# Optimization experiments

Measured on AMD Instinct MI355X. Metric: run time of the kernel, lower is better.

Reference implementation:

```python
import jax, jax.numpy as jnp
import numpy as np

B, M, D = 2048, 1024, 64
NEG_INF = -1e30


def setup_inputs() -> dict:
    key = jax.random.key(0)
    ks = jax.random.split(key, 12)
    s = 0.1  # small init scale for weights
    x = jax.random.normal(ks[0], (B, M, 4), dtype=jnp.float32)
    pad_mask = jax.random.bernoulli(ks[1], 0.1, (B, M))  # True = padded point
    return {
        "x": x,
        "pad_mask": pad_mask,
        "W_in": s * jax.random.normal(ks[2], (4, D), dtype=jnp.float32),
        "b_in": jnp.zeros((D,), jnp.float32),
        "seed": s * jax.random.normal(ks[3], (D,), dtype=jnp.float32),
        "Wq": s * jax.random.normal(ks[4], (D, D), dtype=jnp.float32),
        "Wk": s * jax.random.normal(ks[5], (D, D), dtype=jnp.float32),
        "Wv": s * jax.random.normal(ks[6], (D, D), dtype=jnp.float32),
        "Wo": s * jax.random.normal(ks[7], (D, D), dtype=jnp.float32),
        "b_o": jnp.zeros((D,), jnp.float32),
        "w_loc": s * jax.random.normal(ks[8], (D + 4, 1), dtype=jnp.float32),
        "b_loc": jnp.zeros((1,), jnp.float32),
        "prelu_a": jnp.full((1,), 0.25, jnp.float32),  # PReLU default slope
    }


def _wnet_global(x, pad_mask, W_in, b_in, seed, Wq, Wk, Wv, Wo, b_o):
    # Set-transformer style attention pooling -> one embedding per set [B, D]
    h = x @ W_in + b_in                                  # [B, M, D]
    q = seed @ Wq                                        # [D]
    k = h @ Wk                                           # [B, M, D]
    v = h @ Wv                                           # [B, M, D]
    scores = jnp.einsum("d,bmd->bm", q, k) / jnp.sqrt(jnp.float32(D))
    scores = jnp.where(pad_mask, NEG_INF, scores)
    attn = jax.nn.softmax(scores, axis=-1)               # [B, M]
    pooled = jnp.einsum("bm,bmd->bd", attn, v)           # [B, D]
    return pooled @ Wo + b_o                             # [B, D]


def reference(x, pad_mask, W_in, b_in, seed, Wq, Wk, Wv, Wo, b_o, w_loc, b_loc, prelu_a):
    feat = _wnet_global(x, pad_mask, W_in, b_in, seed, Wq, Wk, Wv, Wo, b_o)  # [B, D]
    # WNet_local: Linear on concat([x, feat]) split into two matmuls (same math,
    # avoids materializing the [B, M, D+4] concat)
    z = x @ w_loc[:4] + (feat @ w_loc[4:])[:, None, :] + b_loc               # [B, M, 1]
    w = jnp.where(z >= 0, z, prelu_a * z)[..., 0]                            # PReLU, [B, M]
    w = jnp.where(pad_mask, 0.0, w)
    # WLS: A = [-los, 1], r = residuals; diag(w) @ A == w[...,None] * A
    A = jnp.concatenate([-x[:, :, 1:4], jnp.ones((B, M, 1), x.dtype)], axis=-1)  # [B, M, 4]
    r = x[:, :, 0:1]                                                             # [B, M, 1]
    WA = w[:, :, None] * A
    Wr = w[:, :, None] * r
    out = (jnp.linalg.pinv(WA) @ Wr)[..., 0]                                     # [B, 4]
    return out
```

## Files before the change

### kernel.cpp

```cpp
#include <hip/hip_runtime.h>
#include <math.h>

#define BB 2048
#define MM 1024
#define DD 64
#define NEG_INF_F (-1e30f)

__device__ __forceinline__ float wredsum(float v) {
#pragma unroll
  for (int o = 32; o > 0; o >>= 1) v += __shfl_down(v, o);
  return v;
}
__device__ __forceinline__ float wredmax(float v) {
#pragma unroll
  for (int o = 32; o > 0; o >>= 1) v = fmaxf(v, __shfl_down(v, o));
  return v;
}

__global__ __launch_bounds__(256) void wls_fused(
    const float* __restrict__ x,
    const int*   __restrict__ pad,
    const float* __restrict__ W_in,
    const float* __restrict__ b_in,
    const float* __restrict__ seed,
    const float* __restrict__ Wq,
    const float* __restrict__ Wk,
    const float* __restrict__ Wv,
    const float* __restrict__ Wo,
    const float* __restrict__ b_o,
    const float* __restrict__ w_loc,
    const float* __restrict__ b_loc,
    const float* __restrict__ prelu_a,
    float* __restrict__ out)
{
  const int tid  = threadIdx.x;
  const int b    = blockIdx.x;
  const int wave = tid >> 6;
  const int lane = tid & 63;

  __shared__ float qv[DD], kqv[DD], hb[DD], pooledv[DD], featv[DD];
  __shared__ float c4s[5];
  __shared__ float rbuf[4][16];
  __shared__ float bcast[8];

  const float4* x4 = (const float4*)(x + (size_t)b * MM * 4);
  float4 xr[4];
  int mk[4];
#pragma unroll
  for (int k2 = 0; k2 < 4; ++k2) {
    xr[k2] = x4[tid + 256 * k2];
    mk[k2] = pad[(size_t)b * MM + tid + 256 * k2];
  }

  if (tid < DD) {
    float acc = 0.f;
    for (int e = 0; e < DD; ++e) acc += seed[e] * Wq[e * DD + tid];
    qv[tid] = acc;
  }
  __syncthreads();
  if (tid < DD) {
    float acc = 0.f;
    for (int d = 0; d < DD; ++d) acc += Wk[tid * DD + d] * qv[d];
    kqv[tid] = acc;
  }
  __syncthreads();
  if (tid < 4) {
    float acc = 0.f;
    for (int e = 0; e < DD; ++e) acc += W_in[tid * DD + e] * kqv[e];
    c4s[tid] = acc;
  } else if (tid == 4) {
    float acc = 0.f;
    for (int e = 0; e < DD; ++e) acc += b_in[e] * kqv[e];
    c4s[4] = acc;
  }
  __syncthreads();

  const float c40 = c4s[0], c41 = c4s[1], c42 = c4s[2], c43 = c4s[3], c0 = c4s[4];

  float sc[4];
  float pmax = -INFINITY;
#pragma unroll
  for (int k2 = 0; k2 < 4; ++k2) {
    float s = (xr[k2].x * c40 + xr[k2].y * c41 + xr[k2].z * c42 + xr[k2].w * c43 + c0) * 0.125f;
    if (mk[k2]) s = NEG_INF_F;
    sc[k2] = s;
    pmax = fmaxf(pmax, s);
  }
  pmax = wredmax(pmax);
  if (lane == 0) rbuf[wave][0] = pmax;
  __syncthreads();
  const float smax = fmaxf(fmaxf(rbuf[0][0], rbuf[1][0]), fmaxf(rbuf[2][0], rbuf[3][0]));
  __syncthreads();

  float se = 0.f, sx0 = 0.f, sx1 = 0.f, sx2 = 0.f, sx3 = 0.f;
#pragma unroll
  for (int k2 = 0; k2 < 4; ++k2) {
    float e = expf(sc[k2] - smax);
    se += e;
    sx0 += e * xr[k2].x; sx1 += e * xr[k2].y; sx2 += e * xr[k2].z; sx3 += e * xr[k2].w;
  }
  {
    float v5[5] = {se, sx0, sx1, sx2, sx3};
#pragma unroll
    for (int j = 0; j < 5; ++j) {
      float r = wredsum(v5[j]);
      if (lane == 0) rbuf[wave][j] = r;
    }
  }
  __syncthreads();
  if (tid < 5) bcast[tid] = rbuf[0][tid] + rbuf[1][tid] + rbuf[2][tid] + rbuf[3][tid];
  __syncthreads();

  if (tid < DD) {
    const float Z = bcast[0];
    const float xb0 = bcast[1] / Z, xb1 = bcast[2] / Z, xb2 = bcast[3] / Z, xb3 = bcast[4] / Z;
    hb[tid] = xb0 * W_in[tid] + xb1 * W_in[DD + tid] + xb2 * W_in[2 * DD + tid] +
              xb3 * W_in[3 * DD + tid] + b_in[tid];
  }
  __syncthreads();
  if (tid < DD) {
    float acc = 0.f;
    for (int e = 0; e < DD; ++e) acc += hb[e] * Wv[e * DD + tid];
    pooledv[tid] = acc;
  }
  __syncthreads();
  if (tid < DD) {
    float acc = 0.f;
    for (int e = 0; e < DD; ++e) acc += pooledv[e] * Wo[e * DD + tid];
    featv[tid] = acc + b_o[tid];
  }
  __syncthreads();
  if (wave == 0) {
    float p = featv[lane] * w_loc[4 + lane];
    p = wredsum(p);
    if (lane == 0) bcast[5] = p + b_loc[0];
  }
  __syncthreads();

  const float sB = bcast[5];
  const float aP = prelu_a[0];
  const float wl0 = w_loc[0], wl1 = w_loc[1], wl2 = w_loc[2], wl3 = w_loc[3];

  float g0 = 0.f, g1 = 0.f, g2 = 0.f, g3 = 0.f, g4 = 0.f, g5 = 0.f, g6 = 0.f,
        g7 = 0.f, g8 = 0.f, g9 = 0.f, r0 = 0.f, r1 = 0.f, r2 = 0.f, r3 = 0.f;
#pragma unroll
  for (int k2 = 0; k2 < 4; ++k2) {
    const float x0 = xr[k2].x, x1 = xr[k2].y, x2 = xr[k2].z, x3 = xr[k2].w;
    float z = x0 * wl0 + x1 * wl1 + x2 * wl2 + x3 * wl3 + sB;
    float w = (z >= 0.f) ? z : aP * z;
    if (mk[k2]) w = 0.f;
    const float w2 = w * w;
    g0 += w2 * x1 * x1; g1 += w2 * x1 * x2; g2 += w2 * x1 * x3; g3 -= w2 * x1;
    g4 += w2 * x2 * x2; g5 += w2 * x2 * x3; g6 -= w2 * x2;
    g7 += w2 * x3 * x3; g8 -= w2 * x3;
    g9 += w2;
    r0 -= w2 * x1 * x0; r1 -= w2 * x2 * x0; r2 -= w2 * x3 * x0; r3 += w2 * x0;
  }
  {
    float vals[14] = {g0, g1, g2, g3, g4, g5, g6, g7, g8, g9, r0, r1, r2, r3};
#pragma unroll
    for (int j = 0; j < 14; ++j) {
      float r = wredsum(vals[j]);
      if (lane == 0) rbuf[wave][j] = r;
    }
  }
  __syncthreads();

  if (tid == 0) {
    double s14[14];
#pragma unroll
    for (int j = 0; j < 14; ++j)
      s14[j] = (double)rbuf[0][j] + (double)rbuf[1][j] +
               (double)rbuf[2][j] + (double)rbuf[3][j];
    double G[4][5];
    G[0][0] = s14[0]; G[0][1] = s14[1]; G[0][2] = s14[2]; G[0][3] = s14[3]; G[0][4] = s14[10];
    G[1][0] = s14[1]; G[1][1] = s14[4]; G[1][2] = s14[5]; G[1][3] = s14[6]; G[1][4] = s14[11];
    G[2][0] = s14[2]; G[2][1] = s14[5]; G[2][2] = s14[7]; G[2][3] = s14[8]; G[2][4] = s14[12];
    G[3][0] = s14[3]; G[3][1] = s14[6]; G[3][2] = s14[8]; G[3][3] = s14[9]; G[3][4] = s14[13];

    for (int c = 0; c < 4; ++c) {
      int p = c; double mv = fabs(G[c][c]);
      for (int rr = c + 1; rr < 4; ++rr)
        if (fabs(G[rr][c]) > mv) { mv = fabs(G[rr][c]); p = rr; }
      if (p != c)
        for (int j = c; j < 5; ++j) { double t = G[c][j]; G[c][j] = G[p][j]; G[p][j] = t; }
      const double inv = 1.0 / G[c][c];
      for (int rr = c + 1; rr < 4; ++rr) {
        const double f = G[rr][c] * inv;
        for (int j = c; j < 5; ++j) G[rr][j] -= f * G[c][j];
      }
    }
    double y[4];
    for (int c = 3; c >= 0; --c) {
      double acc = G[c][4];
      for (int j = c + 1; j < 4; ++j) acc -= G[c][j] * y[j];
      y[c] = acc / G[c][c];
    }
    float4 o;
    o.x = (float)y[0]; o.y = (float)y[1]; o.z = (float)y[2]; o.w = (float)y[3];
    *(float4*)(out + (size_t)b * 4) = o;
  }
}

extern "C" void kernel_launch(void* const* d_in, const int* in_sizes, int n_in,
                              void* d_out, int out_size, void* d_ws, size_t ws_size,
                              hipStream_t stream) {
  const float* x       = (const float*)d_in[0];
  const int*   pad     = (const int*)d_in[1];
  const float* W_in    = (const float*)d_in[2];
  const float* b_in    = (const float*)d_in[3];
  const float* seed    = (const float*)d_in[4];
  const float* Wq      = (const float*)d_in[5];
  const float* Wk      = (const float*)d_in[6];
  const float* Wv      = (const float*)d_in[7];
  const float* Wo      = (const float*)d_in[8];
  const float* b_o     = (const float*)d_in[9];
  const float* w_loc   = (const float*)d_in[10];
  const float* b_loc   = (const float*)d_in[11];
  const float* prelu_a = (const float*)d_in[12];
  float* out = (float*)d_out;

  wls_fused<<<dim3(BB), dim3(256), 0, stream>>>(
      x, pad, W_in, b_in, seed, Wq, Wk, Wv, Wo, b_o, w_loc, b_loc, prelu_a, out);
}
```

Measured before the change: 130.6 us.

## Fold Wv/Wo/w_loc chain into per-set scalar coefficients via associativity

Rewrites the feature-to-local-weight path algebraically. Wo·w_loc and then Wv·that vector are precomputed into four coefficients plus a constant, computed in parallel with the query chain. The per-set scalar sB then becomes a 4-term dot product of the attention-weighted mean of x. This removes three 64x64 matvec stages and four block barriers after the softmax reduction, at the cost of a different floating-point summation order.

```diff
diff --git a/kernel.cpp b/kernel.cpp
--- a/kernel.cpp
+++ b/kernel.cpp
@@ -38,8 +38,8 @@
   const int wave = tid >> 6;
   const int lane = tid & 63;
 
-  __shared__ float qv[DD], kqv[DD], hb[DD], pooledv[DD], featv[DD];
-  __shared__ float c4s[5];
+  __shared__ float qv[DD], kqv[DD], tv[DD], uv[DD];
+  __shared__ float cst[10];
   __shared__ float rbuf[4][16];
   __shared__ float bcast[8];
 
@@ -52,30 +52,47 @@
     mk[k2] = pad[(size_t)b * MM + tid + 256 * k2];
   }
 
-  if (tid < DD) {
-    float acc = 0.f;
-    for (int e = 0; e < DD; ++e) acc += seed[e] * Wq[e * DD + tid];
-    qv[tid] = acc;
-  }
-  __syncthreads();
-  if (tid < DD) {
-    float acc = 0.f;
-    for (int d = 0; d < DD; ++d) acc += Wk[tid * DD + d] * qv[d];
-    kqv[tid] = acc;
+  if (wave == 0) {
+    float acc = 0.f;
+    for (int e = 0; e < DD; ++e) acc += seed[e] * Wq[e * DD + lane];
+    qv[lane] = acc;
+  } else if (wave == 1) {
+    float acc = 0.f;
+    for (int j = 0; j < DD; ++j) acc += Wo[lane * DD + j] * w_loc[4 + j];
+    tv[lane] = acc;
+  }
+  __syncthreads();
+  if (wave == 0) {
+    float acc = 0.f;
+    for (int d = 0; d < DD; ++d) acc += Wk[lane * DD + d] * qv[d];
+    kqv[lane] = acc;
+  } else if (wave == 1) {
+    float acc = 0.f;
+    for (int j = 0; j < DD; ++j) acc += Wv[lane * DD + j] * tv[j];
+    uv[lane] = acc;
   }
   __syncthreads();
   if (tid < 4) {
     float acc = 0.f;
     for (int e = 0; e < DD; ++e) acc += W_in[tid * DD + e] * kqv[e];
-    c4s[tid] = acc;
+    cst[tid] = acc;
   } else if (tid == 4) {
     float acc = 0.f;
     for (int e = 0; e < DD; ++e) acc += b_in[e] * kqv[e];
-    c4s[4] = acc;
-  }
-  __syncthreads();
-
-  const float c40 = c4s[0], c41 = c4s[1], c42 = c4s[2], c43 = c4s[3], c0 = c4s[4];
+    cst[4] = acc;
+  } else if (tid >= 5 && tid < 9) {
+    float acc = 0.f;
+    for (int e = 0; e < DD; ++e) acc += W_in[(tid - 5) * DD + e] * uv[e];
+    cst[tid] = acc;
+  } else if (tid == 9) {
+    float acc = 0.f;
+    for (int e = 0; e < DD; ++e) acc += b_in[e] * uv[e] + b_o[e] * w_loc[4 + e];
+    cst[9] = acc + b_loc[0];
+  }
+  __syncthreads();
+
+  const float c40 = cst[0], c41 = cst[1], c42 = cst[2], c43 = cst[3], c0 = cst[4];
+  const float d40 = cst[5], d41 = cst[6], d42 = cst[7], d43 = cst[8], d0 = cst[9];
 
   float sc[4];
   float pmax = -INFINITY;
@@ -111,33 +128,10 @@
   if (tid < 5) bcast[tid] = rbuf[0][tid] + rbuf[1][tid] + rbuf[2][tid] + rbuf[3][tid];
   __syncthreads();
 
-  if (tid < DD) {
-    const float Z = bcast[0];
-    const float xb0 = bcast[1] / Z, xb1 = bcast[2] / Z, xb2 = bcast[3] / Z, xb3 = bcast[4] / Z;
-    hb[tid] = xb0 * W_in[tid] + xb1 * W_in[DD + tid] + xb2 * W_in[2 * DD + tid] +
-              xb3 * W_in[3 * DD + tid] + b_in[tid];
-  }
-  __syncthreads();
-  if (tid < DD) {
-    float acc = 0.f;
-    for (int e = 0; e < DD; ++e) acc += hb[e] * Wv[e * DD + tid];
-    pooledv[tid] = acc;
-  }
-  __syncthreads();
-  if (tid < DD) {
-    float acc = 0.f;
-    for (int e = 0; e < DD; ++e) acc += pooledv[e] * Wo[e * DD + tid];
-    featv[tid] = acc + b_o[tid];
-  }
-  __syncthreads();
-  if (wave == 0) {
-    float p = featv[lane] * w_loc[4 + lane];
-    p = wredsum(p);
-    if (lane == 0) bcast[5] = p + b_loc[0];
-  }
-  __syncthreads();
-
-  const float sB = bcast[5];
+  const float Z = bcast[0];
+  const float xb0 = bcast[1] / Z, xb1 = bcast[2] / Z, xb2 = bcast[3] / Z, xb3 = bcast[4] / Z;
+  const float sB = xb0 * d40 + xb1 * d41 + xb2 * d42 + xb3 * d43 + d0;
+
   const float aP = prelu_a[0];
   const float wl0 = w_loc[0], wl1 = w_loc[1], wl2 = w_loc[2], wl3 = w_loc[3];
 
```

Measured after the change: 132.3 us. No clear change (+1.3%).
